# Kernel tuning notes

Hardware: AMD Instinct MI355X
Metric: run time of the kernel (lower is better)

The kernel has to match this reference:

```python
import jax, jax.numpy as jnp
import numpy as np

B, S, I, H, C = 32, 512, 768, 512, 10


def setup_inputs() -> dict:
    key = jax.random.key(0)
    ks = jax.random.split(key, 16)
    n = lambda k, shp, s=0.02: jax.random.normal(k, shp, dtype=jnp.float32) * s
    inp = {
        "sentence_embeds": jax.random.normal(ks[0], (B, S, I), dtype=jnp.float32),
        "Wenc": n(ks[1], (H, I)),
        "benc": jnp.zeros((H,), jnp.float32),
        "Wdec": n(ks[2], (H, H)),
        "bdec": jnp.zeros((H,), jnp.float32),
        "v": jax.random.uniform(ks[3], (H,), dtype=jnp.float32),
        "Wih_f": n(ks[4], (4 * H, 2 * I)),
        "Whh_f": n(ks[5], (4 * H, H)),
        "bih_f": jnp.zeros((4 * H,), jnp.float32),
        "bhh_f": jnp.zeros((4 * H,), jnp.float32),
        "Wih_b": n(ks[6], (4 * H, 2 * I)),
        "Whh_b": n(ks[7], (4 * H, H)),
        "bih_b": jnp.zeros((4 * H,), jnp.float32),
        "bhh_b": jnp.zeros((4 * H,), jnp.float32),
        "Wout": n(ks[8], (C, 2 * H)),
        "bout": jnp.zeros((C,), jnp.float32),
    }
    return inp


def _run_direction(embeds, enc_proj, Wdec, bdec, v, Wih, Whh, bih, bhh):
    # embeds: [B,S,I], enc_proj: [B,S,H]. Returns per-step hidden states [S,B,H].
    b = embeds.shape[0]
    h0 = jnp.zeros((b, H), embeds.dtype)
    c0 = jnp.zeros((b, H), embeds.dtype)

    def step(carry, x_t):
        h, c = carry
        # Bahdanau additive attention over all encoder positions
        dec = h @ Wdec.T + bdec                                   # [B,H]
        scores = jnp.einsum("h,bsh->bs", v, jnp.tanh(enc_proj + dec[:, None, :]))
        w = jax.nn.softmax(scores, axis=1)                        # [B,S]
        ctx = jnp.einsum("bs,bsi->bi", w, embeds)                 # [B,I]
        inp = jnp.concatenate([ctx, x_t], axis=1)                 # [B,2I]
        gates = inp @ Wih.T + h @ Whh.T + (bih + bhh)             # [B,4H]
        i, f, g, o = jnp.split(gates, 4, axis=1)                  # torch LSTM gate order
        c = jax.nn.sigmoid(f) * c + jax.nn.sigmoid(i) * jnp.tanh(g)
        h = jax.nn.sigmoid(o) * jnp.tanh(c)
        return (h, c), h

    xs = jnp.swapaxes(embeds, 0, 1)  # [S,B,I]
    _, hs = jax.lax.scan(step, (h0, c0), xs)
    return hs


def reference(sentence_embeds, Wenc, benc, Wdec, bdec, v, Wih_f, Whh_f, bih_f, bhh_f,
              Wih_b, Whh_b, bih_b, bhh_b, Wout, bout):
    # Encoder projection is loop-invariant in the original; compute once.
    enc_proj = sentence_embeds @ Wenc.T + benc  # [B,S,H]
    hs_f = _run_direction(sentence_embeds, enc_proj, Wdec, bdec, v, Wih_f, Whh_f, bih_f, bhh_f)
    hs_b = _run_direction(sentence_embeds[:, ::-1, :], enc_proj, Wdec, bdec, v, Wih_b, Whh_b, bih_b, bhh_b)
    hs_b = hs_b[::-1]                                             # align backward outputs to time order
    combined = jnp.concatenate([hs_f, hs_b], axis=-1)             # [S,B,2H]
    preds = combined @ Wout.T + bout                              # [S,B,C]
    return jnp.swapaxes(preds, 0, 1)                              # [B,S,C]
```

## Files before the change

kernel.cpp:

```cpp
#include <hip/hip_runtime.h>
#include <stdint.h>

#define DEVINL __device__ __forceinline__

constexpr int B_  = 32;
constexpr int S_  = 512;
constexpr int I_  = 768;
constexpr int H_  = 512;
constexpr int C_  = 10;
constexpr int R_  = 64;
constexpr int G4H = 2048;
constexpr int I2_ = 1536;
constexpr int NBLK = 256;
constexpr int NTHR = 512;

using bf16x8 = __attribute__((ext_vector_type(8))) short;
using f32x4  = __attribute__((ext_vector_type(4))) float;
typedef unsigned short u16;
typedef unsigned int   u32;

constexpr size_t OFF_TE   = 0;
constexpr size_t OFF_EMB  = OFF_TE   + (size_t)B_*S_*H_*2;
constexpr size_t OFF_WDEC = OFF_EMB  + (size_t)B_*S_*I_*2;
constexpr size_t OFF_WHH  = OFF_WDEC + (size_t)H_*H_*2;
constexpr size_t OFF_WIL  = OFF_WHH  + (size_t)2*G4H*H_*2;
constexpr size_t OFF_WIR  = OFF_WIL  + (size_t)2*G4H*I_*2;
constexpr size_t OFF_WENC = OFF_WIR  + (size_t)2*G4H*I_*2;
constexpr size_t OFF_H    = OFF_WENC + (size_t)H_*I_*2;
constexpr size_t OFF_C    = OFF_H    + (size_t)R_*H_*2;
constexpr size_t OFF_TD   = OFF_C    + (size_t)R_*H_*4;
constexpr size_t OFF_HWH  = OFF_TD   + (size_t)R_*H_*4;
constexpr size_t OFF_XW   = OFF_HWH  + (size_t)R_*G4H*4;
constexpr size_t OFF_CTX  = OFF_XW   + (size_t)R_*G4H*4;
constexpr size_t OFF_SUME = OFF_CTX  + (size_t)R_*I_*4;
constexpr size_t OFF_M    = OFF_SUME + 256;
constexpr size_t OFF_BAR  = OFF_M    + 256;
constexpr int    BAR_W    = 64 + 32*32;
constexpr size_t WS_NEED  = OFF_BAR + BAR_W*4;

DEVINL float asf(u32 u){ union{u32 i; float f;} x; x.i=u; return x.f; }
DEVINL u32   asu(float f){ union{u32 i; float f;} x; x.f=f; return x.i; }
DEVINL float bf2f(u16 h){ return asf((u32)h << 16); }
DEVINL u16   f2bf(float f){ u32 u = asu(f); return (u16)((u + 0x7fffu + ((u>>16)&1u)) >> 16); }
DEVINL float frcp(float x){
#if __has_builtin(__builtin_amdgcn_rcpf)
  return __builtin_amdgcn_rcpf(x);
#else
  return 1.0f/x;
#endif
}
DEVINL float sigm(float x){ return frcp(1.0f + __expf(-x)); }

DEVINL void gridbar(u32* bar, u32 n){
  __syncthreads();
  if (threadIdx.x == 0){
    __threadfence();
    u32 g = blockIdx.x >> 3;
    u32 old = __hip_atomic_fetch_add(&bar[64 + g*32], 1u, __ATOMIC_RELAXED, __HIP_MEMORY_SCOPE_AGENT);
    if (old == n*8u - 1u){
      u32 r = __hip_atomic_fetch_add(&bar[0], 1u, __ATOMIC_RELAXED, __HIP_MEMORY_SCOPE_AGENT);
      if (r == n*32u - 1u){
        __hip_atomic_store(&bar[32], n, __ATOMIC_RELAXED, __HIP_MEMORY_SCOPE_AGENT);
      }
    }
    while (__hip_atomic_load(&bar[32], __ATOMIC_RELAXED, __HIP_MEMORY_SCOPE_AGENT) < n)
      __builtin_amdgcn_s_sleep(2);
    __threadfence();
  }
  __syncthreads();
}

struct SMemB { float ldsE[2][2][32]; float cpart[192][8]; };
struct SMemC { u16 Abuf[16][776]; float Gpre[4][8][16]; float Gs[4][8][16];
               float Hb[8][16]; float inv[8]; float sum[8]; };
union alignas(16) SMem { SMemB b; SMemC c; };

__global__ void k_setup(char* ws, const float* Wenc, const float* Wdec,
                        const float* Whh_f, const float* Whh_b,
                        const float* Wih_f, const float* Wih_b,
                        float* out){
  int tid = blockIdx.x*blockDim.x + threadIdx.x;
  int nth = gridDim.x*blockDim.x;
  for (int i = tid; i < B_*S_*C_; i += nth) out[i] = 0.f;
  u16* hB = (u16*)(ws+OFF_H);
  for (int i = tid; i < R_*H_; i += nth) hB[i] = 0;
  float* cS = (float*)(ws+OFF_C);
  for (int i = tid; i < R_*H_; i += nth) cS[i] = 0.f;
  float* mb = (float*)(ws+OFF_M);
  for (int i = tid; i < R_; i += nth) mb[i] = 0.f;
  u32* bar = (u32*)(ws+OFF_BAR);
  for (int i = tid; i < BAR_W; i += nth) bar[i] = 0u;
  u16* wd = (u16*)(ws+OFF_WDEC);
  for (int i = tid; i < H_*H_; i += nth) wd[i] = f2bf(Wdec[i]);
  u16* we = (u16*)(ws+OFF_WENC);
  for (int i = tid; i < H_*I_; i += nth) we[i] = f2bf(Wenc[i]);
  u16* wh = (u16*)(ws+OFF_WHH);
  for (int i = tid; i < G4H*H_; i += nth){
    wh[i] = f2bf(Whh_f[i]);
    wh[G4H*H_ + i] = f2bf(Whh_b[i]);
  }
  u16* wl = (u16*)(ws+OFF_WIL);
  u16* wr = (u16*)(ws+OFF_WIR);
  for (int i = tid; i < G4H*I_; i += nth){
    int n = i / I_, k = i - n*I_;
    wl[i]            = f2bf(Wih_f[n*I2_ + k]);
    wr[i]            = f2bf(Wih_f[n*I2_ + I_ + k]);
    wl[G4H*I_ + i]   = f2bf(Wih_b[n*I2_ + k]);
    wr[G4H*I_ + i]   = f2bf(Wih_b[n*I2_ + I_ + k]);
  }
}

__global__ void k_embconv(char* ws, const float* emb){
  u16* e = (u16*)(ws+OFF_EMB);
  int tid = blockIdx.x*blockDim.x + threadIdx.x;
  int nth = gridDim.x*blockDim.x;
  int n4 = (B_*S_*I_)/4;
  const float4* src = (const float4*)emb;
  ushort4* dst = (ushort4*)e;
  for (int i = tid; i < n4; i += nth){
    float4 x = src[i];
    ushort4 o;
    o.x = f2bf(x.x); o.y = f2bf(x.y); o.z = f2bf(x.z); o.w = f2bf(x.w);
    dst[i] = o;
  }
}

__global__ __launch_bounds__(256) void k_enc(char* ws, const float* benc){
  const u16* A = (const u16*)(ws+OFF_EMB);
  const u16* W = (const u16*)(ws+OFF_WENC);
  u16* Te = (u16*)(ws+OFF_TE);
  int wg = blockIdx.x;
  int mt = wg >> 3, ng = wg & 7;
  int wave = threadIdx.x >> 6, lane = threadIdx.x & 63;
  int m0 = mt*16, n0 = ng*64 + wave*16;
  int lr = lane & 15, lkb = (lane>>4)*8;
  const u16* ap = A + (size_t)(m0+lr)*I_ + lkb;
  const u16* bp = W + (size_t)(n0+lr)*I_ + lkb;
  f32x4 acc = {0.f,0.f,0.f,0.f};
  for (int k = 0; k < I_; k += 32){
    bf16x8 a = *(const bf16x8*)(ap + k);
    bf16x8 b = *(const bf16x8*)(bp + k);
    acc = __builtin_amdgcn_mfma_f32_16x16x32_bf16(a, b, acc, 0, 0, 0);
  }
  int row4 = (lane>>4)*4;
  #pragma unroll
  for (int q = 0; q < 4; q++){
    int rr = m0 + row4 + q, cc = n0 + lr;
    Te[(size_t)rr*H_ + cc] = f2bf(tanhf(acc[q] + benc[cc]));
  }
}

__global__ __launch_bounds__(NTHR) void k_persist(char* ws,
        const float* bdec, const float* v,
        const float* bih_f, const float* bhh_f,
        const float* bih_b, const float* bhh_b,
        const float* Wout, const float* bout, float* out){
  __shared__ SMem sh;
  __shared__ u16 embLds[64][I_];
  u32* bar = (u32*)(ws+OFF_BAR);
  u32 gen = 0;
  const int tid = threadIdx.x, lane = tid & 63, wave = tid >> 6;
  const int lr = lane & 15, lkb = (lane>>4)*8, row4 = (lane>>4)*4;

  const int ab   = blockIdx.x & 31;
  const int pair = blockIdx.x >> 5;
  const int s0A  = pair*32, s0B = S_ - pair*32 - 32;
  const int h0   = lane*8;

  for (int i = tid; i < 16*776; i += NTHR) ((u16*)sh.c.Abuf)[i] = 0;

  {
    const u16* E = (const u16*)(ws+OFF_EMB);
    for (int idx = tid; idx < 64*(I_/8); idx += NTHR){
      int r = idx / (I_/8), c8 = idx - r*(I_/8);
      int s = (r < 32) ? (s0A + r) : (s0B + (r-32));
      *(uint4*)(&embLds[r][c8*8]) = *(const uint4*)(E + ((size_t)(ab*S_ + s))*I_ + c8*8);
    }
  }
  bf16x8 teR[8];
  {
    const u16* Te = (const u16*)(ws+OFF_TE);
    #pragma unroll
    for (int k = 0; k < 8; ++k){
      int r = wave + 8*k;
      int ci = r >> 5, u = r & 31;
      int s = (ci ? s0B : s0A) + u;
      teR[k] = *(const bf16x8*)(Te + ((size_t)(ab*S_ + s))*H_ + h0);
    }
  }
  __syncthreads();

  for (int t = 0; t < S_; ++t){
    {
      int gw = blockIdx.x*8 + wave;
      const u16* hB = (const u16*)(ws+OFF_H);
      if (gw < 128){
        int m0 = (gw>>5)*16, n0 = (gw&31)*16;
        const u16* W = (const u16*)(ws+OFF_WDEC);
        const u16* ap = hB + (size_t)(m0+lr)*H_ + lkb;
        const u16* bp = W + (size_t)(n0+lr)*H_ + lkb;
        f32x4 acc = {0.f,0.f,0.f,0.f};
        for (int k = 0; k < H_; k += 32){
          bf16x8 a = *(const bf16x8*)(ap + k);
          bf16x8 b = *(const bf16x8*)(bp + k);
          acc = __builtin_amdgcn_mfma_f32_16x16x32_bf16(a, b, acc, 0, 0, 0);
        }
        float* Td = (float*)(ws+OFF_TD);
        #pragma unroll
        for (int q = 0; q < 4; q++){
          int rr = m0 + row4 + q, cc = n0 + lr;
          Td[rr*H_ + cc] = tanhf(acc[q] + bdec[cc]);
        }
      } else if (gw < 640){
        int t2 = gw - 128; int dir = t2 >> 8; int t3 = t2 & 255;
        int m0 = dir*32 + (t3>>7)*16;
        int n0 = (t3 & 127)*16;
        const u16* W = (const u16*)(ws+OFF_WHH) + (size_t)dir*G4H*H_;
        const u16* ap = hB + (size_t)(m0+lr)*H_ + lkb;
        const u16* bp = W + (size_t)(n0+lr)*H_ + lkb;
        f32x4 acc = {0.f,0.f,0.f,0.f};
        for (int k = 0; k < H_; k += 32){
          bf16x8 a = *(const bf16x8*)(ap + k);
          bf16x8 b = *(const bf16x8*)(bp + k);
          acc = __builtin_amdgcn_mfma_f32_16x16x32_bf16(a, b, acc, 0, 0, 0);
        }
        float* o = (float*)(ws+OFF_HWH);
        #pragma unroll
        for (int q = 0; q < 4; q++){
          int rr = m0 + row4 + q;
          o[(size_t)rr*G4H + n0 + lr] = acc[q];
        }
      } else if (gw < 1152){
        int t2 = gw - 640; int dir = t2 >> 8; int t3 = t2 & 255;
        int bbase = (t3>>7)*16;
        int n0 = (t3 & 127)*16;
        int trow = dir ? (S_-1-t) : t;
        const u16* E = (const u16*)(ws+OFF_EMB);
        const u16* W = (const u16*)(ws+OFF_WIR) + (size_t)dir*G4H*I_;
        const u16* ap = E + ((size_t)(bbase+lr)*S_ + trow)*I_ + lkb;
        const u16* bp = W + (size_t)(n0+lr)*I_ + lkb;
        f32x4 acc = {0.f,0.f,0.f,0.f};
        for (int k = 0; k < I_; k += 32){
          bf16x8 a = *(const bf16x8*)(ap + k);
          bf16x8 b = *(const bf16x8*)(bp + k);
          acc = __builtin_amdgcn_mfma_f32_16x16x32_bf16(a, b, acc, 0, 0, 0);
        }
        float* o = (float*)(ws+OFF_XW);
        #pragma unroll
        for (int q = 0; q < 4; q++){
          int bb = bbase + row4 + q;
          o[(size_t)(dir*32+bb)*G4H + n0 + lr] = acc[q];
        }
      } else {
        int zid = (gw - 1152)*64 + lane;
        float* ctx = (float*)(ws+OFF_CTX);
        if (zid < R_*I_) ctx[zid] = 0.f;
        if (zid < R_) ((float*)(ws+OFF_SUME))[zid] = 0.f;
      }
    }
    gridbar(bar, ++gen);
    {
      const float* Td = (const float*)(ws+OFF_TD);
      const float* mbp = (const float*)(ws+OFF_M);
      float tdf[8], tdb[8], va[8];
      #pragma unroll
      for (int j = 0; j < 8; j++){
        tdf[j] = Td[ab*H_ + h0 + j];
        tdb[j] = Td[(32+ab)*H_ + h0 + j];
        va[j]  = v[h0 + j];
      }
      float mF = mbp[ab], mB = mbp[32+ab];
      #pragma unroll
      for (int k = 0; k < 8; ++k){
        int r = wave + 8*k;
        int ci = r >> 5, u = r & 31;
        bf16x8 tv = teR[k];
        float af = 0.f, ab2 = 0.f;
        #pragma unroll
        for (int j = 0; j < 8; ++j){
          float te = bf2f((u16)tv[j]);
          float df = fmaf(te, tdf[j], 1.0f);
          float db = fmaf(te, tdb[j], 1.0f);
          af  = fmaf((te+tdf[j])*frcp(df), va[j], af);
          ab2 = fmaf((te+tdb[j])*frcp(db), va[j], ab2);
        }
        #pragma unroll
        for (int off = 1; off < 64; off <<= 1){
          af  += __shfl_xor(af, off);
          ab2 += __shfl_xor(ab2, off);
        }
        float ef = __expf(fminf(fmaxf(af  - mF, -80.f), 80.f));
        float eb = __expf(fminf(fmaxf(ab2 - mB, -80.f), 80.f));
        if (lane == 0){ sh.b.ldsE[0][ci][u] = ef; sh.b.ldsE[1][ci][u] = eb; }
      }
      __syncthreads();
      if (tid < 2){
        float s = 0.f;
        for (int ci = 0; ci < 2; ci++)
          for (int u = 0; u < 32; u++) s += sh.b.ldsE[tid][ci][u];
        atomicAdd((float*)(ws+OFF_SUME) + tid*32 + ab, s);
      }
      float cf[4] = {0.f,0.f,0.f,0.f}, cb[4] = {0.f,0.f,0.f,0.f};
      if (tid < 384){
        int hf = (tid >= 192) ? 1 : 0;
        int t2 = hf ? tid-192 : tid;
        int i0 = t2*4;
        #pragma unroll 4
        for (int u = 0; u < 32; u++){
          ushort4 x4 = *(const ushort4*)(&embLds[hf*32 + u][i0]);
          float wf = sh.b.ldsE[0][hf][u];
          float wb = sh.b.ldsE[1][1-hf][31-u];
          float x0 = bf2f(x4.x), x1 = bf2f(x4.y), x2 = bf2f(x4.z), x3 = bf2f(x4.w);
          cf[0] = fmaf(wf, x0, cf[0]); cf[1] = fmaf(wf, x1, cf[1]);
          cf[2] = fmaf(wf, x2, cf[2]); cf[3] = fmaf(wf, x3, cf[3]);
          cb[0] = fmaf(wb, x0, cb[0]); cb[1] = fmaf(wb, x1, cb[1]);
          cb[2] = fmaf(wb, x2, cb[2]); cb[3] = fmaf(wb, x3, cb[3]);
        }
        if (hf){
          #pragma unroll
          for (int z = 0; z < 4; z++){
            sh.b.cpart[t2][z]   = cf[z];
            sh.b.cpart[t2][4+z] = cb[z];
          }
        }
      }
      __syncthreads();
      if (tid < 192){
        float* ctx = (float*)(ws+OFF_CTX);
        int i0 = tid*4;
        #pragma unroll
        for (int z = 0; z < 4; z++){
          atomicAdd(&ctx[(size_t)ab*I_ + i0 + z],      cf[z] + sh.b.cpart[tid][z]);
          atomicAdd(&ctx[(size_t)(32+ab)*I_ + i0 + z], cb[z] + sh.b.cpart[tid][4+z]);
        }
      }
    }
    gridbar(bar, ++gen);
    {
      int blk = blockIdx.x;
      int dir = blk >> 7, rest = blk & 127, hc = rest >> 2, qb = rest & 3;
      int rb0 = qb*8;
      const float* se = (const float*)(ws+OFF_SUME) + dir*32;
      if (tid < 8){
        float s_ = se[rb0 + tid];
        sh.c.sum[tid] = s_;
        sh.c.inv[tid] = 1.0f / fmaxf(s_, 1e-30f);
      }
      __syncthreads();
      const float* ctx = (const float*)(ws+OFF_CTX) + (size_t)dir*32*I_;
      for (int idx = tid; idx < 8*I_; idx += NTHR){
        int j = idx / I_, k = idx - j*I_;
        sh.c.Abuf[j][k] = f2bf(ctx[(size_t)(rb0+j)*I_ + k] * sh.c.inv[j]);
      }
      __syncthreads();
      f32x4 acc = {0.f,0.f,0.f,0.f};
      if (wave < 4){
        int gt = wave;
        const u16* Wp = (const u16*)(ws+OFF_WIL) + (size_t)dir*G4H*I_;
        int n_g = gt*512 + hc*16 + lr;
        const u16* bp = Wp + (size_t)n_g*I_ + lkb;
        for (int k = 0; k < I_; k += 32){
          bf16x8 av = *(const bf16x8*)(&sh.c.Abuf[lr][k + lkb]);
          bf16x8 bv = *(const bf16x8*)(bp + k);
          acc = __builtin_amdgcn_mfma_f32_16x16x32_bf16(av, bv, acc, 0, 0, 0);
        }
      } else {
        int gt = wave - 4;
        const float* xW = (const float*)(ws+OFF_XW);
        const float* hW = (const float*)(ws+OFF_HWH);
        const float* bih = dir ? bih_b : bih_f;
        const float* bhh = dir ? bhh_b : bhh_f;
        int j0 = lane >> 4, col = lane & 15;
        int n = gt*512 + hc*16 + col;
        #pragma unroll
        for (int jj = j0; jj < 8; jj += 4){
          size_t rr = (size_t)(dir*32 + rb0 + jj);
          sh.c.Gpre[gt][jj][col] = xW[rr*G4H + n] + hW[rr*G4H + n] + bih[n] + bhh[n];
        }
      }
      __syncthreads();
      if (wave < 4){
        int gt = wave, col = lane & 15;
        #pragma unroll
        for (int q = 0; q < 4; q++){
          int row = row4 + q;
          if (row < 8) sh.c.Gs[gt][row][col] = acc[q] + sh.c.Gpre[gt][row][col];
        }
      }
      __syncthreads();
      float* cS = (float*)(ws+OFF_C);
      u16* hBw = (u16*)(ws+OFF_H);
      if (tid < 128){
        int j = tid >> 4, col = tid & 15;
        int hg = hc*16 + col;
        size_t rr = (size_t)(dir*32 + rb0 + j);
        float ig = sigm(sh.c.Gs[0][j][col]);
        float fg = sigm(sh.c.Gs[1][j][col]);
        float gg = tanhf(sh.c.Gs[2][j][col]);
        float og = sigm(sh.c.Gs[3][j][col]);
        float cn = fmaf(fg, cS[rr*H_ + hg], ig*gg);
        float hn = og * tanhf(cn);
        cS[rr*H_ + hg] = cn;
        hBw[rr*H_ + hg] = f2bf(hn);
        sh.c.Hb[j][col] = hn;
      }
      __syncthreads();
      if (tid < 80){
        int bb = tid/10, cc = tid - bb*10;
        const float* wr = Wout + (size_t)cc*1024 + dir*512 + hc*16;
        float s = 0.f;
        #pragma unroll
        for (int j = 0; j < 16; j++) s = fmaf(sh.c.Hb[bb][j], wr[j], s);
        if (dir == 0 && hc == 0) s += bout[cc];
        int st = dir ? (S_-1-t) : t;
        atomicAdd(&out[((size_t)(qb*8+bb)*S_ + st)*C_ + cc], s);
      }
      if (hc == 0 && tid < 8){
        float* mbp = (float*)(ws+OFF_M);
        mbp[dir*32 + rb0 + tid] += logf(fmaxf(sh.c.sum[tid], 1e-30f));
      }
    }
    gridbar(bar, ++gen);
  }
}

extern "C" void kernel_launch(void* const* d_in, const int* in_sizes, int n_in,
                              void* d_out, int out_size, void* d_ws, size_t ws_size,
                              hipStream_t stream){
  const float* emb   = (const float*)d_in[0];
  const float* Wenc  = (const float*)d_in[1];
  const float* benc  = (const float*)d_in[2];
  const float* Wdec  = (const float*)d_in[3];
  const float* bdec  = (const float*)d_in[4];
  const float* v     = (const float*)d_in[5];
  const float* Wih_f = (const float*)d_in[6];
  const float* Whh_f = (const float*)d_in[7];
  const float* bih_f = (const float*)d_in[8];
  const float* bhh_f = (const float*)d_in[9];
  const float* Wih_b = (const float*)d_in[10];
  const float* Whh_b = (const float*)d_in[11];
  const float* bih_b = (const float*)d_in[12];
  const float* bhh_b = (const float*)d_in[13];
  const float* Wout  = (const float*)d_in[14];
  const float* bout  = (const float*)d_in[15];
  float* out = (float*)d_out;
  char* ws = (char*)d_ws;
  if (ws_size < WS_NEED) return;

  k_setup<<<dim3(512), dim3(256), 0, stream>>>(ws, Wenc, Wdec, Whh_f, Whh_b, Wih_f, Wih_b, out);
  k_embconv<<<dim3(2048), dim3(256), 0, stream>>>(ws, emb);
  k_enc<<<dim3(8192), dim3(256), 0, stream>>>(ws, benc);
  k_persist<<<dim3(NBLK), dim3(NTHR), 0, stream>>>(ws, bdec, v,
      bih_f, bhh_f, bih_b, bhh_b, Wout, bout, out);
}
```

Before: 28.56 ms.

## Pin per-block weight slices in LDS and embeddings in registers across timesteps

```diff
diff --git a/kernel.cpp b/kernel.cpp
--- a/kernel.cpp
+++ b/kernel.cpp
@@ -70,9 +70,9 @@
   __syncthreads();
 }
 
-struct SMemB { float ldsE[2][2][32]; float cpart[192][8]; };
-struct SMemC { u16 Abuf[16][776]; float Gpre[4][8][16]; float Gs[4][8][16];
-               float Hb[8][16]; float inv[8]; float sum[8]; };
+struct SMemB { float ldsE[2][2][32]; float cpart[4][96][16]; };
+struct SMemC { u16 Abuf[16][776]; float Gpre[32][16]; float Gs[32][16];
+               float Hb[16][8]; float inv[16]; float sum[16]; };
 union alignas(16) SMem { SMemB b; SMemC c; };
 
 __global__ void k_setup(char* ws, const float* Wenc, const float* Wdec,
@@ -156,103 +156,110 @@
         const float* bih_b, const float* bhh_b,
         const float* Wout, const float* bout, float* out){
   __shared__ SMem sh;
-  __shared__ u16 embLds[64][I_];
+  __shared__ alignas(16) u16 wWhh[16][520];
+  __shared__ alignas(16) u16 wWIR[16][776];
+  __shared__ alignas(16) u16 wDec[16][520];
+  __shared__ alignas(16) u16 wWIL[32][776];
+  __shared__ float wOutL[10][8];
+  __shared__ float bsumL[32];
   u32* bar = (u32*)(ws+OFF_BAR);
   u32 gen = 0;
   const int tid = threadIdx.x, lane = tid & 63, wave = tid >> 6;
   const int lr = lane & 15, lkb = (lane>>4)*8, row4 = (lane>>4)*4;
-
-  const int ab   = blockIdx.x & 31;
-  const int pair = blockIdx.x >> 5;
+  const int blk = blockIdx.x;
+  const int dirA = blk & 1, n0A = blk >> 1;
+  const int ab   = blk & 31, pair = blk >> 5;
   const int s0A  = pair*32, s0B = S_ - pair*32 - 32;
   const int h0   = lane*8;
-
-  for (int i = tid; i < 16*776; i += NTHR) ((u16*)sh.c.Abuf)[i] = 0;
-
-  {
-    const u16* E = (const u16*)(ws+OFF_EMB);
-    for (int idx = tid; idx < 64*(I_/8); idx += NTHR){
-      int r = idx / (I_/8), c8 = idx - r*(I_/8);
-      int s = (r < 32) ? (s0A + r) : (s0B + (r-32));
-      *(uint4*)(&embLds[r][c8*8]) = *(const uint4*)(E + ((size_t)(ab*S_ + s))*I_ + c8*8);
-    }
-  }
+  const int cg   = (tid < 384) ? (tid % 96) : 0;
+  const int rq   = (tid < 384) ? (tid / 96) : 0;
+  const int dirC = blk >> 7, ncC = (blk >> 1) & 63, qbC = blk & 1;
+
+  { const u16* src = (const u16*)(ws+OFF_WHH) + (size_t)dirA*G4H*H_ + (size_t)n0A*16*H_;
+    for (int idx = tid; idx < 16*64; idx += NTHR){ int r = idx>>6, c8 = idx&63;
+      *(uint4*)&wWhh[r][c8*8] = *(const uint4*)(src + (size_t)r*H_ + c8*8); } }
+  { const u16* src = (const u16*)(ws+OFF_WIR) + (size_t)dirA*G4H*I_ + (size_t)n0A*16*I_;
+    for (int idx = tid; idx < 16*96; idx += NTHR){ int r = idx/96, c8 = idx - r*96;
+      *(uint4*)&wWIR[r][c8*8] = *(const uint4*)(src + (size_t)r*I_ + c8*8); } }
+  if (blk < 32){
+    const u16* src = (const u16*)(ws+OFF_WDEC) + (size_t)blk*16*H_;
+    for (int idx = tid; idx < 16*64; idx += NTHR){ int r = idx>>6, c8 = idx&63;
+      *(uint4*)&wDec[r][c8*8] = *(const uint4*)(src + (size_t)r*H_ + c8*8); } }
+  { const u16* src = (const u16*)(ws+OFF_WIL) + (size_t)dirC*G4H*I_;
+    for (int idx = tid; idx < 32*96; idx += NTHR){ int pr = idx/96, c8 = idx - pr*96;
+      int g = pr>>3, j = pr&7;
+      *(uint4*)&wWIL[pr][c8*8] = *(const uint4*)(src + (size_t)(g*512 + ncC*8 + j)*I_ + c8*8); } }
+  { const float* bihp = dirC ? bih_b : bih_f;
+    const float* bhhp = dirC ? bhh_b : bhh_f;
+    if (tid < 32){ int g = tid>>3, c = tid&7; int n = g*512 + ncC*8 + c;
+      bsumL[tid] = bihp[n] + bhhp[n]; }
+    if (tid >= 64 && tid < 144){ int q = tid-64; int cc = q>>3, c = q&7;
+      wOutL[cc][c] = Wout[(size_t)cc*1024 + dirC*512 + ncC*8 + c]; } }
   bf16x8 teR[8];
-  {
-    const u16* Te = (const u16*)(ws+OFF_TE);
+  { const u16* Te = (const u16*)(ws+OFF_TE);
     #pragma unroll
     for (int k = 0; k < 8; ++k){
-      int r = wave + 8*k;
-      int ci = r >> 5, u = r & 31;
+      int r = wave + 8*k; int ci = r >> 5, u = r & 31;
       int s = (ci ? s0B : s0A) + u;
-      teR[k] = *(const bf16x8*)(Te + ((size_t)(ab*S_ + s))*H_ + h0);
-    }
-  }
+      teR[k] = *(const bf16x8*)(Te + ((size_t)(ab*S_ + s))*H_ + h0); } }
+  bf16x8 embR[16];
+  if (tid < 384){
+    const u16* E = (const u16*)(ws+OFF_EMB);
+    #pragma unroll
+    for (int j = 0; j < 16; ++j){
+      int r = rq*16 + j;
+      int s = (r < 32) ? (s0A + r) : (s0B + (r - 32));
+      embR[j] = *(const bf16x8*)(E + ((size_t)(ab*S_ + s))*I_ + cg*8); } }
   __syncthreads();
 
   for (int t = 0; t < S_; ++t){
     {
-      int gw = blockIdx.x*8 + wave;
       const u16* hB = (const u16*)(ws+OFF_H);
-      if (gw < 128){
-        int m0 = (gw>>5)*16, n0 = (gw&31)*16;
-        const u16* W = (const u16*)(ws+OFF_WDEC);
+      if (wave < 2){
+        int m0 = dirA*32 + wave*16;
         const u16* ap = hB + (size_t)(m0+lr)*H_ + lkb;
-        const u16* bp = W + (size_t)(n0+lr)*H_ + lkb;
         f32x4 acc = {0.f,0.f,0.f,0.f};
         for (int k = 0; k < H_; k += 32){
           bf16x8 a = *(const bf16x8*)(ap + k);
-          bf16x8 b = *(const bf16x8*)(bp + k);
+          bf16x8 b = *(const bf16x8*)(&wWhh[lr][k + lkb]);
           acc = __builtin_amdgcn_mfma_f32_16x16x32_bf16(a, b, acc, 0, 0, 0);
         }
-        float* Td = (float*)(ws+OFF_TD);
-        #pragma unroll
-        for (int q = 0; q < 4; q++){
-          int rr = m0 + row4 + q, cc = n0 + lr;
-          Td[rr*H_ + cc] = tanhf(acc[q] + bdec[cc]);
-        }
-      } else if (gw < 640){
-        int t2 = gw - 128; int dir = t2 >> 8; int t3 = t2 & 255;
-        int m0 = dir*32 + (t3>>7)*16;
-        int n0 = (t3 & 127)*16;
-        const u16* W = (const u16*)(ws+OFF_WHH) + (size_t)dir*G4H*H_;
+        float* o = (float*)(ws+OFF_HWH);
+        #pragma unroll
+        for (int q = 0; q < 4; q++)
+          o[(size_t)(m0 + row4 + q)*G4H + n0A*16 + lr] = acc[q];
+      } else if (wave < 4){
+        int bbase = (wave-2)*16;
+        int trow = dirA ? (S_-1-t) : t;
+        const u16* E = (const u16*)(ws+OFF_EMB);
+        const u16* ap = E + ((size_t)(bbase+lr)*S_ + trow)*I_ + lkb;
+        f32x4 acc = {0.f,0.f,0.f,0.f};
+        for (int k = 0; k < I_; k += 32){
+          bf16x8 a = *(const bf16x8*)(ap + k);
+          bf16x8 b = *(const bf16x8*)(&wWIR[lr][k + lkb]);
+          acc = __builtin_amdgcn_mfma_f32_16x16x32_bf16(a, b, acc, 0, 0, 0);
+        }
+        float* o = (float*)(ws+OFF_XW);
+        #pragma unroll
+        for (int q = 0; q < 4; q++)
+          o[(size_t)(dirA*32 + bbase + row4 + q)*G4H + n0A*16 + lr] = acc[q];
+      } else if (blk < 32){
+        int m0 = (wave-4)*16;
         const u16* ap = hB + (size_t)(m0+lr)*H_ + lkb;
-        const u16* bp = W + (size_t)(n0+lr)*H_ + lkb;
         f32x4 acc = {0.f,0.f,0.f,0.f};
         for (int k = 0; k < H_; k += 32){
           bf16x8 a = *(const bf16x8*)(ap + k);
-          bf16x8 b = *(const bf16x8*)(bp + k);
+          bf16x8 b = *(const bf16x8*)(&wDec[lr][k + lkb]);
           acc = __builtin_amdgcn_mfma_f32_16x16x32_bf16(a, b, acc, 0, 0, 0);
         }
-        float* o = (float*)(ws+OFF_HWH);
+        float* Td = (float*)(ws+OFF_TD);
         #pragma unroll
         for (int q = 0; q < 4; q++){
-          int rr = m0 + row4 + q;
-          o[(size_t)rr*G4H + n0 + lr] = acc[q];
-        }
-      } else if (gw < 1152){
-        int t2 = gw - 640; int dir = t2 >> 8; int t3 = t2 & 255;
-        int bbase = (t3>>7)*16;
-        int n0 = (t3 & 127)*16;
-        int trow = dir ? (S_-1-t) : t;
-        const u16* E = (const u16*)(ws+OFF_EMB);
-        const u16* W = (const u16*)(ws+OFF_WIR) + (size_t)dir*G4H*I_;
-        const u16* ap = E + ((size_t)(bbase+lr)*S_ + trow)*I_ + lkb;
-        const u16* bp = W + (size_t)(n0+lr)*I_ + lkb;
-        f32x4 acc = {0.f,0.f,0.f,0.f};
-        for (int k = 0; k < I_; k += 32){
-          bf16x8 a = *(const bf16x8*)(ap + k);
-          bf16x8 b = *(const bf16x8*)(bp + k);
-          acc = __builtin_amdgcn_mfma_f32_16x16x32_bf16(a, b, acc, 0, 0, 0);
-        }
-        float* o = (float*)(ws+OFF_XW);
-        #pragma unroll
-        for (int q = 0; q < 4; q++){
-          int bb = bbase + row4 + q;
-          o[(size_t)(dir*32+bb)*G4H + n0 + lr] = acc[q];
+          int rr = m0 + row4 + q, cc = blk*16 + lr;
+          Td[rr*H_ + cc] = tanhf(acc[q] + bdec[cc]);
         }
       } else {
-        int zid = (gw - 1152)*64 + lane;
+        int zid = (((blk-32)<<2) + (wave-4))*64 + lane;
         float* ctx = (float*)(ws+OFF_CTX);
         if (zid < R_*I_) ctx[zid] = 0.f;
         if (zid < R_) ((float*)(ws+OFF_SUME))[zid] = 0.f;
@@ -300,124 +307,114 @@
           for (int u = 0; u < 32; u++) s += sh.b.ldsE[tid][ci][u];
         atomicAdd((float*)(ws+OFF_SUME) + tid*32 + ab, s);
       }
-      float cf[4] = {0.f,0.f,0.f,0.f}, cb[4] = {0.f,0.f,0.f,0.f};
       if (tid < 384){
-        int hf = (tid >= 192) ? 1 : 0;
-        int t2 = hf ? tid-192 : tid;
-        int i0 = t2*4;
-        #pragma unroll 4
-        for (int u = 0; u < 32; u++){
-          ushort4 x4 = *(const ushort4*)(&embLds[hf*32 + u][i0]);
-          float wf = sh.b.ldsE[0][hf][u];
-          float wb = sh.b.ldsE[1][1-hf][31-u];
-          float x0 = bf2f(x4.x), x1 = bf2f(x4.y), x2 = bf2f(x4.z), x3 = bf2f(x4.w);
-          cf[0] = fmaf(wf, x0, cf[0]); cf[1] = fmaf(wf, x1, cf[1]);
-          cf[2] = fmaf(wf, x2, cf[2]); cf[3] = fmaf(wf, x3, cf[3]);
-          cb[0] = fmaf(wb, x0, cb[0]); cb[1] = fmaf(wb, x1, cb[1]);
-          cb[2] = fmaf(wb, x2, cb[2]); cb[3] = fmaf(wb, x3, cb[3]);
-        }
-        if (hf){
+        const int ci = rq >> 1;
+        float cf[8] = {0,0,0,0,0,0,0,0}, cb[8] = {0,0,0,0,0,0,0,0};
+        #pragma unroll
+        for (int j = 0; j < 16; ++j){
+          int u = ((rq & 1) << 4) + j;
+          float wf = sh.b.ldsE[0][ci][u];
+          float wb = sh.b.ldsE[1][1-ci][31-u];
+          bf16x8 e = embR[j];
           #pragma unroll
-          for (int z = 0; z < 4; z++){
-            sh.b.cpart[t2][z]   = cf[z];
-            sh.b.cpart[t2][4+z] = cb[z];
+          for (int x = 0; x < 8; ++x){
+            float ev = bf2f((u16)e[x]);
+            cf[x] = fmaf(wf, ev, cf[x]);
+            cb[x] = fmaf(wb, ev, cb[x]);
           }
         }
-      }
-      __syncthreads();
-      if (tid < 192){
-        float* ctx = (float*)(ws+OFF_CTX);
-        int i0 = tid*4;
-        #pragma unroll
-        for (int z = 0; z < 4; z++){
-          atomicAdd(&ctx[(size_t)ab*I_ + i0 + z],      cf[z] + sh.b.cpart[tid][z]);
-          atomicAdd(&ctx[(size_t)(32+ab)*I_ + i0 + z], cb[z] + sh.b.cpart[tid][4+z]);
+        #pragma unroll
+        for (int x = 0; x < 8; ++x){
+          sh.b.cpart[rq][cg][x]   = cf[x];
+          sh.b.cpart[rq][cg][8+x] = cb[x];
+        }
+      }
+      __syncthreads();
+      {
+        float* ctxg = (float*)(ws+OFF_CTX);
+        for (int o = tid; o < 1536; o += NTHR){
+          int d = (o >= 768) ? 1 : 0;
+          int col = o - d*768;
+          int cgx = col >> 3, c = col & 7;
+          float s = sh.b.cpart[0][cgx][d*8+c] + sh.b.cpart[1][cgx][d*8+c]
+                  + sh.b.cpart[2][cgx][d*8+c] + sh.b.cpart[3][cgx][d*8+c];
+          atomicAdd(&ctxg[(size_t)(d*32+ab)*I_ + col], s);
         }
       }
     }
     gridbar(bar, ++gen);
     {
-      int blk = blockIdx.x;
-      int dir = blk >> 7, rest = blk & 127, hc = rest >> 2, qb = rest & 3;
-      int rb0 = qb*8;
-      const float* se = (const float*)(ws+OFF_SUME) + dir*32;
-      if (tid < 8){
-        float s_ = se[rb0 + tid];
+      const float* se = (const float*)(ws+OFF_SUME) + dirC*32 + qbC*16;
+      if (tid < 16){
+        float s_ = se[tid];
         sh.c.sum[tid] = s_;
         sh.c.inv[tid] = 1.0f / fmaxf(s_, 1e-30f);
       }
       __syncthreads();
-      const float* ctx = (const float*)(ws+OFF_CTX) + (size_t)dir*32*I_;
-      for (int idx = tid; idx < 8*I_; idx += NTHR){
+      const float* ctx = (const float*)(ws+OFF_CTX) + (size_t)(dirC*32 + qbC*16)*I_;
+      for (int idx = tid; idx < 16*I_; idx += NTHR){
         int j = idx / I_, k = idx - j*I_;
-        sh.c.Abuf[j][k] = f2bf(ctx[(size_t)(rb0+j)*I_ + k] * sh.c.inv[j]);
+        sh.c.Abuf[j][k] = f2bf(ctx[(size_t)j*I_ + k] * sh.c.inv[j]);
       }
       __syncthreads();
       f32x4 acc = {0.f,0.f,0.f,0.f};
-      if (wave < 4){
-        int gt = wave;
-        const u16* Wp = (const u16*)(ws+OFF_WIL) + (size_t)dir*G4H*I_;
-        int n_g = gt*512 + hc*16 + lr;
-        const u16* bp = Wp + (size_t)n_g*I_ + lkb;
+      if (wave < 2){
         for (int k = 0; k < I_; k += 32){
           bf16x8 av = *(const bf16x8*)(&sh.c.Abuf[lr][k + lkb]);
-          bf16x8 bv = *(const bf16x8*)(bp + k);
+          bf16x8 bv = *(const bf16x8*)(&wWIL[wave*16 + lr][k + lkb]);
           acc = __builtin_amdgcn_mfma_f32_16x16x32_bf16(av, bv, acc, 0, 0, 0);
         }
       } else {
-        int gt = wave - 4;
         const float* xW = (const float*)(ws+OFF_XW);
         const float* hW = (const float*)(ws+OFF_HWH);
-        const float* bih = dir ? bih_b : bih_f;
-        const float* bhh = dir ? bhh_b : bhh_f;
-        int j0 = lane >> 4, col = lane & 15;
-        int n = gt*512 + hc*16 + col;
-        #pragma unroll
-        for (int jj = j0; jj < 8; jj += 4){
-          size_t rr = (size_t)(dir*32 + rb0 + jj);
-          sh.c.Gpre[gt][jj][col] = xW[rr*G4H + n] + hW[rr*G4H + n] + bih[n] + bhh[n];
-        }
-      }
-      __syncthreads();
-      if (wave < 4){
-        int gt = wave, col = lane & 15;
+        for (int ii = tid - 128; ii < 512; ii += 384){
+          int pr = ii >> 4, j = ii & 15;
+          int g = pr >> 3, c = pr & 7;
+          int n = g*512 + ncC*8 + c;
+          size_t rr = (size_t)(dirC*32 + qbC*16 + j);
+          sh.c.Gpre[pr][j] = xW[rr*G4H + n] + hW[rr*G4H + n] + bsumL[pr];
+        }
+      }
+      __syncthreads();
+      if (wave < 2){
+        int pr = wave*16 + lr;
         #pragma unroll
         for (int q = 0; q < 4; q++){
-          int row = row4 + q;
-          if (row < 8) sh.c.Gs[gt][row][col] = acc[q] + sh.c.Gpre[gt][row][col];
+          int j = row4 + q;
+          sh.c.Gs[pr][j] = acc[q] + sh.c.Gpre[pr][j];
         }
       }
       __syncthreads();
       float* cS = (float*)(ws+OFF_C);
       u16* hBw = (u16*)(ws+OFF_H);
       if (tid < 128){
-        int j = tid >> 4, col = tid & 15;
-        int hg = hc*16 + col;
-        size_t rr = (size_t)(dir*32 + rb0 + j);
-        float ig = sigm(sh.c.Gs[0][j][col]);
-        float fg = sigm(sh.c.Gs[1][j][col]);
-        float gg = tanhf(sh.c.Gs[2][j][col]);
-        float og = sigm(sh.c.Gs[3][j][col]);
+        int j = tid >> 3, c = tid & 7;
+        int hg = ncC*8 + c;
+        size_t rr = (size_t)(dirC*32 + qbC*16 + j);
+        float ig = sigm(sh.c.Gs[c][j]);
+        float fg = sigm(sh.c.Gs[8+c][j]);
+        float gg = tanhf(sh.c.Gs[16+c][j]);
+        float og = sigm(sh.c.Gs[24+c][j]);
         float cn = fmaf(fg, cS[rr*H_ + hg], ig*gg);
         float hn = og * tanhf(cn);
         cS[rr*H_ + hg] = cn;
         hBw[rr*H_ + hg] = f2bf(hn);
-        sh.c.Hb[j][col] = hn;
-      }
-      __syncthreads();
-      if (tid < 80){
-        int bb = tid/10, cc = tid - bb*10;
-        const float* wr = Wout + (size_t)cc*1024 + dir*512 + hc*16;
+        sh.c.Hb[j][c] = hn;
+      }
+      __syncthreads();
+      if (tid < 160){
+        int j = tid/10, cc = tid - j*10;
         float s = 0.f;
         #pragma unroll
-        for (int j = 0; j < 16; j++) s = fmaf(sh.c.Hb[bb][j], wr[j], s);
-        if (dir == 0 && hc == 0) s += bout[cc];
-        int st = dir ? (S_-1-t) : t;
-        atomicAdd(&out[((size_t)(qb*8+bb)*S_ + st)*C_ + cc], s);
-      }
-      if (hc == 0 && tid < 8){
+        for (int c = 0; c < 8; c++) s = fmaf(sh.c.Hb[j][c], wOutL[cc][c], s);
+        if (dirC == 0 && ncC == 0) s += bout[cc];
+        int bb = qbC*16 + j;
+        int st = dirC ? (S_-1-t) : t;
+        atomicAdd(&out[((size_t)bb*S_ + st)*C_ + cc], s);
+      }
+      if (ncC == 0 && tid < 16){
         float* mbp = (float*)(ws+OFF_M);
-        mbp[dir*32 + rb0 + tid] += logf(fmaxf(sh.c.sum[tid], 1e-30f));
+        mbp[dirC*32 + qbC*16 + tid] += logf(fmaxf(sh.c.sum[tid], 1e-30f));
       }
     }
     gridbar(bar, ++gen);
```

Measured after the change: 27.48 ms. 1.04x faster.
